# Kernel optimization log

Hardware: AMD Instinct MI355X
Metric: run time of the kernel (lower is better)

## Reference

```python
import jax, jax.numpy as jnp
import numpy as np

EDGES = np.array([[0,13],[0,1],[0,4],[0,10],[0,7],[13,14],[14,15],[15,16],[1,2],[2,3],
                  [3,17],[4,5],[5,6],[6,18],[10,11],[11,12],[12,19],[7,8],[8,9],[9,20]])
N = 21
EPS = 1e-5


def _build_adj():
    # adj_mx_from_edges: symmetric binary adjacency + self-loops, row-normalized (D^-1 (A+I))
    A = np.zeros((N, N), np.float32)
    A[EDGES[:, 0], EDGES[:, 1]] = 1.0
    A = np.maximum(A, A.T)
    A = A + np.eye(N, dtype=np.float32)
    A = A / A.sum(1, keepdims=True)
    return A


def setup_inputs() -> dict:
    key = jax.random.key(0)
    ks = jax.random.split(key, 10)
    B, C, H, W = 64, 256, 64, 64
    s = 0.05
    return {
        "feature_s": jax.random.normal(ks[0], (B, C, H, W), jnp.float32),
        "target_s": jax.random.uniform(ks[1], (B, N, H, W), jnp.float32),
        "adj": jnp.asarray(_build_adj()),
        "bn_gamma": jnp.ones((N,), jnp.float32),
        "bn_beta": jnp.zeros((N,), jnp.float32),
        "gru_wx": s * jax.random.normal(ks[2], (256, 768), jnp.float32),
        "gru_wh": s * jax.random.normal(ks[3], (256, 768), jnp.float32),
        "gru_bx": jnp.zeros((768,), jnp.float32),
        "gru_bh": jnp.zeros((768,), jnp.float32),
        "w_g1": s * jax.random.normal(ks[4], (2, 256, 256), jnp.float32),
        "b_g1": jnp.zeros((256,), jnp.float32),
        "w_g2": s * jax.random.normal(ks[5], (2, 256, 256), jnp.float32),
        "b_g2": jnp.zeros((256,), jnp.float32),
        "w_out": s * jax.random.normal(ks[6], (2, 256, 3), jnp.float32),
        "b_out": jnp.zeros((3,), jnp.float32),
    }


def _batchnorm1d(x, gamma, beta):
    # x: [B, 21, C]; BatchNorm1d over channel dim 21 (stats over batch and length)
    mean = jnp.mean(x, axis=(0, 2), keepdims=True)
    var = jnp.var(x, axis=(0, 2), keepdims=True)
    xn = (x - mean) * jax.lax.rsqrt(var + EPS)
    return xn * gamma[None, :, None] + beta[None, :, None]


def _gru(x, wx, wh, bx, bh):
    # standard GRU scanned over the 21-joint axis; x: [B, N, 256] -> [B, N, 256]
    B, n, Hd = x.shape
    xg = jnp.einsum('bnc,ch->bnh', x, wx) + bx  # [B, N, 3H]

    def step(h, xg_t):
        hg = h @ wh + bh
        r = jax.nn.sigmoid(xg_t[..., :Hd] + hg[..., :Hd])
        z = jax.nn.sigmoid(xg_t[..., Hd:2 * Hd] + hg[..., Hd:2 * Hd])
        ncand = jnp.tanh(xg_t[..., 2 * Hd:] + r * hg[..., 2 * Hd:])
        h_new = (1.0 - z) * ncand + z * h
        return h_new, h_new

    h0 = jnp.zeros((B, Hd), x.dtype)
    _, ys = jax.lax.scan(step, h0, jnp.swapaxes(xg, 0, 1))
    return jnp.swapaxes(ys, 0, 1)


def _laplacian(adj):
    # normalized Laplacian L = I - D^{-1/2} A D^{-1/2}
    d = adj.sum(-1)
    dinv = jnp.where(d > 0, jax.lax.rsqrt(jnp.where(d > 0, d, 1.0)), 0.0)
    return jnp.eye(N, dtype=adj.dtype) - dinv[:, None] * adj * dinv[None, :]


def _chebconv(x, L, w, b):
    # K=2 Chebyshev conv: T0 = I, T1 = L ->  x @ W0 + (L x) @ W1 + b
    return jnp.einsum('bnc,co->bno', x, w[0]) + jnp.einsum('nm,bmc,co->bno', L, x, w[1]) + b


def reference(feature_s, target_s, adj, bn_gamma, bn_beta,
              gru_wx, gru_wh, gru_bx, gru_bh,
              w_g1, b_g1, w_g2, b_g2, w_out, b_out):
    B, C, H, W = feature_s.shape
    # batched correlation: [B, 21, HW] x [B, HW, C] -> [B, 21, C]
    q = jnp.einsum('bjp,bcp->bjc',
                   target_s.reshape(B, N, H * W),
                   feature_s.reshape(B, C, H * W))
    q = _batchnorm1d(q, bn_gamma, bn_beta)
    q = jnp.where(q > 0, q, 0.1 * q)  # LeakyReLU(0.1)
    q = _gru(q, gru_wx, gru_wh, gru_bx, gru_bh)
    # _ResChebGC: two graph convs with ReLU + residual (dropout = identity in eval)
    L = _laplacian(adj)
    h = jax.nn.relu(_chebconv(q, L, w_g1, b_g1))
    h = jax.nn.relu(_chebconv(h, L, w_g2, b_g2))
    x = q + h
    return _chebconv(x, L, w_out, b_out)  # [B, 21, 3]
```

## Files before the change

kernel.cpp:

```cpp
#include <hip/hip_runtime.h>
#include <cstdint>

#define B   64
#define NJ  21
#define CHN 256
#define HW  4096
#define G3  768

typedef _Float16 f16x8 __attribute__((ext_vector_type(8)));
typedef float    f32x4 __attribute__((ext_vector_type(4)));
typedef _Float16 f16x2 __attribute__((ext_vector_type(2)));
typedef __fp16   fp16x2v __attribute__((ext_vector_type(2)));
union PKU { fp16x2v h; unsigned u; };
union HU { unsigned u; f16x2 h; };

static __device__ inline unsigned pack_f16(float a, float b){
  HU u; u.h.x = (_Float16)a; u.h.y = (_Float16)b; return u.u;
}

__global__ __launch_bounds__(64) void k_lap(const float* __restrict__ adj, float* __restrict__ L){
  __shared__ float dinv[NJ];
  int t = threadIdx.x;
  if (t < NJ){
    float s = 0.f;
    for (int j=0;j<NJ;j++) s += adj[t*NJ+j];
    dinv[t] = s > 0.f ? 1.f/sqrtf(s) : 0.f;
  }
  __syncthreads();
  for (int idx=t; idx<NJ*NJ; idx+=64){
    int i = idx/NJ, j = idx%NJ;
    L[idx] = (i==j ? 1.f : 0.f) - dinv[i]*adj[idx]*dinv[j];
  }
}

__global__ __launch_bounds__(256,4) void k_corr3(const float* __restrict__ T,
    const float* __restrict__ F, _Float16* __restrict__ P){
  int bid = blockIdx.x;
  int nb = bid & 3, b = (bid>>2)&63, kb = bid>>8;
  int t = threadIdx.x;
  int w = t>>6, l = t&63;
  __shared__ __align__(16) unsigned short At[2][32*64];
  __shared__ __align__(16) unsigned short Bt[2][64*64];

  for (int i=t; i<704; i+=256){
    int bi = (i>=352) ? 1 : 0; int r2 = i - bi*352;
    int r = 21 + (r2>>5); int kk = r2 & 31;
    *(unsigned*)((char*)&At[bi][0] + r*128 + kk*4) = 0u;
  }

  bool isF = (t < 128);
  bool isT = (t >= 128) && (t < 170);
  const float4* gp = nullptr; int srow = 0, shalf = 0;
  if (isF){
    srow = t>>1; shalf = t&1;
    gp = (const float4*)(F + ((size_t)b*CHN + nb*64 + srow)*HW + (size_t)kb*1024) + shalf*8;
  } else if (isT){
    int tt = t-128; srow = tt>>1; shalf = tt&1;
    gp = (const float4*)(T + ((size_t)b*NJ + srow)*HW + (size_t)kb*1024) + shalf*8;
  }
  float4 ld[8];
  if (gp){
    #pragma unroll
    for (int i=0;i<8;i++) ld[i] = gp[i];
  }

  f32x4 acc0 = {0.f,0.f,0.f,0.f}, acc1 = {0.f,0.f,0.f,0.f};
  int arow0 = (l&15);
  int brow  = w*16 + (l&15);
  int kbyt  = (l>>4)*16;

  for (int s=0; s<16; ++s){
    int bi = s & 1;
    if (gp){
      unsigned short* tile = isF ? &Bt[bi][0] : &At[bi][0];
      #pragma unroll
      for (int q=0;q<4;q++){
        PKU p0, p1, p2, p3;
        p0.h = __builtin_amdgcn_cvt_pkrtz(ld[2*q].x,   ld[2*q].y);
        p1.h = __builtin_amdgcn_cvt_pkrtz(ld[2*q].z,   ld[2*q].w);
        p2.h = __builtin_amdgcn_cvt_pkrtz(ld[2*q+1].x, ld[2*q+1].y);
        p3.h = __builtin_amdgcn_cvt_pkrtz(ld[2*q+1].z, ld[2*q+1].w);
        int addr = (srow*128 + shalf*64 + q*16) ^ ((srow&7)<<4);
        uint4 v; v.x = p0.u; v.y = p1.u; v.z = p2.u; v.w = p3.u;
        *(uint4*)((char*)tile + addr) = v;
      }
      if (s < 15){
        const float4* gn = gp + (size_t)(s+1)*16;
        #pragma unroll
        for (int i=0;i<8;i++) ld[i] = gn[i];
      }
    }
    asm volatile("s_waitcnt lgkmcnt(0)\n\ts_barrier" ::: "memory");
    #pragma unroll
    for (int kc=0;kc<2;kc++){
      int kb2 = kc*64 + kbyt;
      int ab0 = ((arow0)*128    + kb2) ^ ((arow0&7)<<4);
      int ab1 = ((arow0+16)*128 + kb2) ^ ((arow0&7)<<4);
      int bb  = ((brow)*128     + kb2) ^ ((brow&7)<<4);
      f16x8 a0 = *(const f16x8*)((const char*)&At[bi][0] + ab0);
      f16x8 a1 = *(const f16x8*)((const char*)&At[bi][0] + ab1);
      f16x8 bf = *(const f16x8*)((const char*)&Bt[bi][0] + bb);
      acc0 = __builtin_amdgcn_mfma_f32_16x16x32_f16(a0, bf, acc0, 0, 0, 0);
      acc1 = __builtin_amdgcn_mfma_f32_16x16x32_f16(a1, bf, acc1, 0, 0, 0);
    }
  }

  int cbase = nb*64 + w*16 + (l&15);
  #pragma unroll
  for (int r=0;r<4;r++){
    int row0 = (l>>4)*4 + r;
    if (row0 < 21)
      P[(((size_t)kb*64 + b)*21 + row0)*256 + cbase] = (_Float16)acc0[r];
    int row1 = row0 + 16;
    if (row1 < 21)
      P[(((size_t)kb*64 + b)*21 + row1)*256 + cbase] = (_Float16)acc1[r];
  }
}

__global__ __launch_bounds__(256) void k_stats(const _Float16* __restrict__ P,
    float* __restrict__ q, float* __restrict__ stats){
  int j = blockIdx.x, t = threadIdx.x;
  const size_t KSTRIDE = (size_t)64*21*256;
  float s = 0.f, ss = 0.f;
  for (int b=0;b<B;b++){
    size_t i0 = ((size_t)b*21 + j)*256 + t;
    float v = (float)P[i0] + (float)P[KSTRIDE + i0]
            + (float)P[2*KSTRIDE + i0] + (float)P[3*KSTRIDE + i0];
    q[((size_t)b*NJ + j)*CHN + t] = v;
    s += v; ss += v*v;
  }
  #pragma unroll
  for (int o=32;o>0;o>>=1){ s += __shfl_down(s,o); ss += __shfl_down(ss,o); }
  __shared__ float sb[4], ssb[4];
  int wid = t>>6;
  if ((t&63)==0){ sb[wid]=s; ssb[wid]=ss; }
  __syncthreads();
  if (t==0){
    float S  = sb[0]+sb[1]+sb[2]+sb[3];
    float SS = ssb[0]+ssb[1]+ssb[2]+ssb[3];
    float mean = S * (1.f/16384.f);
    float var  = SS * (1.f/16384.f) - mean*mean;
    stats[j]      = mean;
    stats[NJ + j] = 1.f/sqrtf(var + 1e-5f);
  }
}

__global__ __launch_bounds__(256) void k_xg(const float* __restrict__ q,
    const float* __restrict__ stats, const float* __restrict__ gamma, const float* __restrict__ beta,
    const float* __restrict__ wx, const float* __restrict__ bx, float* __restrict__ xg){
  int b = blockIdx.x/3, sl = blockIdx.x%3;
  int t = threadIdx.x;
  int col = sl*256 + t;
  __shared__ float xn[NJ][CHN];
  for (int idx=t; idx<NJ*CHN; idx+=256){
    int j = idx >> 8;
    float v = (q[(size_t)b*NJ*CHN + idx] - stats[j]) * stats[NJ+j];
    v = v * gamma[j] + beta[j];
    xn[j][idx & 255] = v > 0.f ? v : 0.1f*v;
  }
  __syncthreads();
  float acc[NJ];
  #pragma unroll
  for (int j=0;j<NJ;j++) acc[j]=0.f;
  for (int c=0;c<CHN;c++){
    float wv = wx[(size_t)c*G3 + col];
    #pragma unroll
    for (int j=0;j<NJ;j++) acc[j] += xn[j][c]*wv;
  }
  float bv = bx[col];
  #pragma unroll
  for (int j=0;j<NJ;j++) xg[((size_t)b*NJ+j)*G3 + col] = acc[j] + bv;
}

__global__ __launch_bounds__(256) void k_pack2(const float* __restrict__ wh, unsigned* __restrict__ whp2){
  int idx = blockIdx.x*256 + threadIdx.x;
  int col = idx >> 7, c2 = idx & 127;
  float w0 = wh[(size_t)(2*c2)*G3 + col];
  float w1 = wh[(size_t)(2*c2+1)*G3 + col];
  whp2[idx] = pack_f16(w0, w1);
}

__global__ __launch_bounds__(768,3) void k_gru(const unsigned* __restrict__ whp2,
    const float* __restrict__ bh, const float* __restrict__ xg, float* __restrict__ gout){
  int b = blockIdx.x;
  int col = threadIdx.x;
  int l = col & 63;
  __shared__ float hf[256];
  __shared__ float lr[256], lz[256];
  const uint4* wp = (const uint4*)(whp2 + (size_t)col*128);
  float bhv = bh[col];
  if (col < 256) hf[col] = 0.f;
  unsigned hv0 = 0u, hv1 = 0u;
  float xv_next = xg[((size_t)b*NJ + 0)*G3 + col];
  __syncthreads();
  for (int step=0; step<NJ; ++step){
    float xvc = xv_next;
    if (step < NJ-1) xv_next = xg[((size_t)b*NJ + step+1)*G3 + col];
    float a = 0.f;
    #pragma unroll
    for (int i=0;i<32;i++){
      uint4 v = wp[i];
      HU w, h;
#if __has_builtin(__builtin_amdgcn_fdot2)
      w.u=v.x; h.u=__builtin_amdgcn_readlane(i<16?hv0:hv1, (4*i)&63);   a=__builtin_amdgcn_fdot2(w.h,h.h,a,false);
      w.u=v.y; h.u=__builtin_amdgcn_readlane(i<16?hv0:hv1, (4*i+1)&63); a=__builtin_amdgcn_fdot2(w.h,h.h,a,false);
      w.u=v.z; h.u=__builtin_amdgcn_readlane(i<16?hv0:hv1, (4*i+2)&63); a=__builtin_amdgcn_fdot2(w.h,h.h,a,false);
      w.u=v.w; h.u=__builtin_amdgcn_readlane(i<16?hv0:hv1, (4*i+3)&63); a=__builtin_amdgcn_fdot2(w.h,h.h,a,false);
#else
      w.u=v.x; h.u=__builtin_amdgcn_readlane(i<16?hv0:hv1, (4*i)&63);   a+=(float)w.h.x*(float)h.h.x+(float)w.h.y*(float)h.h.y;
      w.u=v.y; h.u=__builtin_amdgcn_readlane(i<16?hv0:hv1, (4*i+1)&63); a+=(float)w.h.x*(float)h.h.x+(float)w.h.y*(float)h.h.y;
      w.u=v.z; h.u=__builtin_amdgcn_readlane(i<16?hv0:hv1, (4*i+2)&63); a+=(float)w.h.x*(float)h.h.x+(float)w.h.y*(float)h.h.y;
      w.u=v.w; h.u=__builtin_amdgcn_readlane(i<16?hv0:hv1, (4*i+3)&63); a+=(float)w.h.x*(float)h.h.x+(float)w.h.y*(float)h.h.y;
#endif
    }
    a += bhv;
    if (col < 256)      lr[col]     = 1.f/(1.f+__expf(-(xvc + a)));
    else if (col < 512) lz[col-256] = 1.f/(1.f+__expf(-(xvc + a)));
    __syncthreads();
    if (col >= 512){
      int i = col - 512;
      float nv = tanhf(xvc + lr[i]*a);
      float z  = lz[i];
      float hnew = (1.f - z)*nv + z*hf[i];
      gout[((size_t)b*NJ + step)*CHN + i] = hnew;
      hf[i] = hnew;
    }
    __syncthreads();
    float2 p0 = *(const float2*)&hf[2*l];
    float2 p1 = *(const float2*)&hf[128 + 2*l];
    hv0 = pack_f16(p0.x, p0.y);
    hv1 = pack_f16(p1.x, p1.y);
  }
}

__global__ __launch_bounds__(256) void k_cheb(const float* __restrict__ xin,
    const float* __restrict__ Lm, const float* __restrict__ W,
    const float* __restrict__ bvec, float* __restrict__ out){
  int b = blockIdx.x >> 2, oq = blockIdx.x & 3;
  int t = threadIdx.x;
  int ol = t & 63, ck = t >> 6;
  __shared__ float xs[NJ][CHN];
  __shared__ float lx[NJ][CHN];
  __shared__ float part[4][64][NJ];
  for (int idx=t; idx<NJ*CHN; idx+=256) xs[idx>>8][idx&255] = xin[(size_t)b*NJ*CHN + idx];
  __syncthreads();
  for (int idx=t; idx<NJ*CHN; idx+=256){
    int j = idx>>8, c = idx&255;
    float sacc = 0.f;
    #pragma unroll
    for (int m=0;m<NJ;m++) sacc += Lm[j*NJ+m]*xs[m][c];
    lx[j][c] = sacc;
  }
  __syncthreads();
  int o = oq*64 + ol;
  float acc[NJ];
  #pragma unroll
  for (int j=0;j<NJ;j++) acc[j]=0.f;
  const float* W0 = W;
  const float* W1 = W + CHN*CHN;
  for (int cc=0; cc<64; ++cc){
    int c = ck*64 + cc;
    float w0 = W0[(size_t)c*CHN + o];
    float w1 = W1[(size_t)c*CHN + o];
    #pragma unroll
    for (int j=0;j<NJ;j++){ acc[j] += xs[j][c]*w0; acc[j] += lx[j][c]*w1; }
  }
  #pragma unroll
  for (int j=0;j<NJ;j++) part[ck][ol][j] = acc[j];
  __syncthreads();
  for (int idx=t; idx<64*NJ; idx+=256){
    int o2 = idx & 63, j = idx >> 6;
    float s2 = part[0][o2][j]+part[1][o2][j]+part[2][o2][j]+part[3][o2][j] + bvec[oq*64+o2];
    s2 = s2 > 0.f ? s2 : 0.f;
    out[(size_t)b*NJ*CHN + j*CHN + oq*64 + o2] = s2;
  }
}

__global__ __launch_bounds__(64) void k_out(const float* __restrict__ gq, const float* __restrict__ h2,
    const float* __restrict__ Lm, const float* __restrict__ W, const float* __restrict__ bvec,
    float* __restrict__ out){
  int b = blockIdx.x, t = threadIdx.x;
  __shared__ float xs[NJ][CHN];
  __shared__ float lx[NJ][CHN];
  for (int idx=t; idx<NJ*CHN; idx+=64)
    xs[idx>>8][idx&255] = gq[(size_t)b*NJ*CHN+idx] + h2[(size_t)b*NJ*CHN+idx];
  __syncthreads();
  for (int idx=t; idx<NJ*CHN; idx+=64){
    int j = idx>>8, c = idx&255;
    float s = 0.f;
    #pragma unroll
    for (int m=0;m<NJ;m++) s += Lm[j*NJ+m]*xs[m][c];
    lx[j][c] = s;
  }
  __syncthreads();
  if (t < 63){
    int j = t/3, o = t%3;
    float acc = bvec[o];
    const float* W0 = W;
    const float* W1 = W + CHN*3;
    for (int c=0;c<CHN;c++){
      acc += xs[j][c]*W0[c*3+o];
      acc += lx[j][c]*W1[c*3+o];
    }
    out[(size_t)b*63 + t] = acc;
  }
}

extern "C" void kernel_launch(void* const* d_in, const int* in_sizes, int n_in,
                              void* d_out, int out_size, void* d_ws, size_t ws_size,
                              hipStream_t stream){
  const float* feat  = (const float*)d_in[0];
  const float* targ  = (const float*)d_in[1];
  const float* adj   = (const float*)d_in[2];
  const float* gamma = (const float*)d_in[3];
  const float* beta  = (const float*)d_in[4];
  const float* wx    = (const float*)d_in[5];
  const float* wh    = (const float*)d_in[6];
  const float* bx    = (const float*)d_in[7];
  const float* bh    = (const float*)d_in[8];
  const float* wg1   = (const float*)d_in[9];
  const float* bg1   = (const float*)d_in[10];
  const float* wg2   = (const float*)d_in[11];
  const float* bg2   = (const float*)d_in[12];
  const float* wout  = (const float*)d_in[13];
  const float* bout  = (const float*)d_in[14];

  float* ws   = (float*)d_ws;
  float* q     = ws + 0;
  float* stats = ws + 400000;
  float* Lw    = ws + 400128;
  float* xgw   = ws + 500000;
  float* gout  = ws + 1600000;
  float* h1    = ws + 2000000;
  float* h2b   = ws + 2400000;
  unsigned* whp2 = (unsigned*)(ws + 2800000);
  _Float16* P  = (_Float16*)(ws + 3000000);

  k_lap  <<<1,    64, 0, stream>>>(adj, Lw);
  k_pack2<<<384, 256, 0, stream>>>(wh, whp2);
  k_corr3<<<1024,256, 0, stream>>>(targ, feat, P);
  k_stats<<<21,  256, 0, stream>>>(P, q, stats);
  k_xg   <<<192, 256, 0, stream>>>(q, stats, gamma, beta, wx, bx, xgw);
  k_gru  <<<64,  768, 0, stream>>>(whp2, bh, xgw, gout);
  k_cheb <<<256, 256, 0, stream>>>(gout, Lw, wg1, bg1, h1);
  k_cheb <<<256, 256, 0, stream>>>(h1,   Lw, wg2, bg2, h2b);
  k_out  <<<64,   64, 0, stream>>>(gout, h2b, Lw, wout, bout, (float*)d_out);
}
```

Before: 278.7 us.

## Keep half of GRU recurrent weights in registers, transpose packed layout

Result: faster. 269.6 us (-3.2%).

```diff
diff --git a/kernel.cpp b/kernel.cpp
--- a/kernel.cpp
+++ b/kernel.cpp
@@ -16,6 +16,15 @@
 
 static __device__ inline unsigned pack_f16(float a, float b){
   HU u; u.h.x = (_Float16)a; u.h.y = (_Float16)b; return u.u;
+}
+
+static __device__ inline float fdot2f(unsigned wu, unsigned hu, float acc){
+  HU w, h; w.u = wu; h.u = hu;
+#if __has_builtin(__builtin_amdgcn_fdot2)
+  return __builtin_amdgcn_fdot2(w.h, h.h, acc, false);
+#else
+  return acc + (float)w.h.x*(float)h.h.x + (float)w.h.y*(float)h.h.y;
+#endif
 }
 
 __global__ __launch_bounds__(64) void k_lap(const float* __restrict__ adj, float* __restrict__ L){
@@ -172,22 +181,25 @@
   for (int j=0;j<NJ;j++) xg[((size_t)b*NJ+j)*G3 + col] = acc[j] + bv;
 }
 
-__global__ __launch_bounds__(256) void k_pack2(const float* __restrict__ wh, unsigned* __restrict__ whp2){
+__global__ __launch_bounds__(256) void k_pack(const float* __restrict__ wh, unsigned* __restrict__ whp){
   int idx = blockIdx.x*256 + threadIdx.x;
-  int col = idx >> 7, c2 = idx & 127;
+  int c2 = idx / G3, col = idx % G3;
   float w0 = wh[(size_t)(2*c2)*G3 + col];
   float w1 = wh[(size_t)(2*c2+1)*G3 + col];
-  whp2[idx] = pack_f16(w0, w1);
-}
-
-__global__ __launch_bounds__(768,3) void k_gru(const unsigned* __restrict__ whp2,
+  whp[idx] = pack_f16(w0, w1);
+}
+
+__global__ __launch_bounds__(768,3) void k_gru(const unsigned* __restrict__ whp,
     const float* __restrict__ bh, const float* __restrict__ xg, float* __restrict__ gout){
   int b = blockIdx.x;
   int col = threadIdx.x;
   int l = col & 63;
   __shared__ float hf[256];
   __shared__ float lr[256], lz[256];
-  const uint4* wp = (const uint4*)(whp2 + (size_t)col*128);
+  unsigned wr[64];
+  #pragma unroll
+  for (int i=0;i<64;i++) wr[i] = whp[i*G3 + col];
+  const unsigned* wsp = whp + 64*G3 + col;
   float bhv = bh[col];
   if (col < 256) hf[col] = 0.f;
   unsigned hv0 = 0u, hv1 = 0u;
@@ -196,24 +208,14 @@
   for (int step=0; step<NJ; ++step){
     float xvc = xv_next;
     if (step < NJ-1) xv_next = xg[((size_t)b*NJ + step+1)*G3 + col];
-    float a = 0.f;
-    #pragma unroll
-    for (int i=0;i<32;i++){
-      uint4 v = wp[i];
-      HU w, h;
-#if __has_builtin(__builtin_amdgcn_fdot2)
-      w.u=v.x; h.u=__builtin_amdgcn_readlane(i<16?hv0:hv1, (4*i)&63);   a=__builtin_amdgcn_fdot2(w.h,h.h,a,false);
-      w.u=v.y; h.u=__builtin_amdgcn_readlane(i<16?hv0:hv1, (4*i+1)&63); a=__builtin_amdgcn_fdot2(w.h,h.h,a,false);
-      w.u=v.z; h.u=__builtin_amdgcn_readlane(i<16?hv0:hv1, (4*i+2)&63); a=__builtin_amdgcn_fdot2(w.h,h.h,a,false);
-      w.u=v.w; h.u=__builtin_amdgcn_readlane(i<16?hv0:hv1, (4*i+3)&63); a=__builtin_amdgcn_fdot2(w.h,h.h,a,false);
-#else
-      w.u=v.x; h.u=__builtin_amdgcn_readlane(i<16?hv0:hv1, (4*i)&63);   a+=(float)w.h.x*(float)h.h.x+(float)w.h.y*(float)h.h.y;
-      w.u=v.y; h.u=__builtin_amdgcn_readlane(i<16?hv0:hv1, (4*i+1)&63); a+=(float)w.h.x*(float)h.h.x+(float)w.h.y*(float)h.h.y;
-      w.u=v.z; h.u=__builtin_amdgcn_readlane(i<16?hv0:hv1, (4*i+2)&63); a+=(float)w.h.x*(float)h.h.x+(float)w.h.y*(float)h.h.y;
-      w.u=v.w; h.u=__builtin_amdgcn_readlane(i<16?hv0:hv1, (4*i+3)&63); a+=(float)w.h.x*(float)h.h.x+(float)w.h.y*(float)h.h.y;
-#endif
-    }
-    a += bhv;
+    float a0 = 0.f, a1 = 0.f;
+    #pragma unroll
+    for (int i=0;i<64;i++)
+      a1 = fdot2f(wsp[(size_t)i*G3], __builtin_amdgcn_readlane(hv1, i), a1);
+    #pragma unroll
+    for (int i=0;i<64;i++)
+      a0 = fdot2f(wr[i], __builtin_amdgcn_readlane(hv0, i), a0);
+    float a = a0 + a1 + bhv;
     if (col < 256)      lr[col]     = 1.f/(1.f+__expf(-(xvc + a)));
     else if (col < 512) lz[col-256] = 1.f/(1.f+__expf(-(xvc + a)));
     __syncthreads();
@@ -333,15 +335,15 @@
   float* gout  = ws + 1600000;
   float* h1    = ws + 2000000;
   float* h2b   = ws + 2400000;
-  unsigned* whp2 = (unsigned*)(ws + 2800000);
+  unsigned* whp = (unsigned*)(ws + 2800000);
   _Float16* P  = (_Float16*)(ws + 3000000);
 
   k_lap  <<<1,    64, 0, stream>>>(adj, Lw);
-  k_pack2<<<384, 256, 0, stream>>>(wh, whp2);
+  k_pack <<<384, 256, 0, stream>>>(wh, whp);
   k_corr3<<<1024,256, 0, stream>>>(targ, feat, P);
   k_stats<<<21,  256, 0, stream>>>(P, q, stats);
   k_xg   <<<192, 256, 0, stream>>>(q, stats, gamma, beta, wx, bx, xgw);
-  k_gru  <<<64,  768, 0, stream>>>(whp2, bh, xgw, gout);
+  k_gru  <<<64,  768, 0, stream>>>(whp, bh, xgw, gout);
   k_cheb <<<256, 256, 0, stream>>>(gout, Lw, wg1, bg1, h1);
   k_cheb <<<256, 256, 0, stream>>>(h1,   Lw, wg2, bg2, h2b);
   k_out  <<<64,   64, 0, stream>>>(gout, h2b, Lw, wout, bout, (float*)d_out);
```
